# Kernel tuning notes

Hardware: AMD Instinct MI355X
Metric: run time of the kernel (lower is better)

Reference implementation:

```python
import jax, jax.numpy as jnp
import numpy as np

F = 65536          # num_face
W_DIM = 512
PAD = 4096         # zero pad rows appended before gather
LRELU_SLOPE = 0.2
LRELU_GAIN = np.sqrt(2.0).astype(np.float32)  # def_gain of lrelu


def _fc(w, W, b):
    # StyleGAN FullyConnectedLayer: x @ W.T / sqrt(in_features) + bias
    gain = np.float32(1.0 / np.sqrt(W.shape[1]))
    return w @ W.T * gain + b


def _faceconv_gather(x, neigh, is_pad, k):
    # x: [B*F, C]; neigh/is_pad: [B*F, 9]; take first k neighbor slots.
    padded = jnp.concatenate([x, jnp.zeros((PAD, x.shape[1]), x.dtype)], axis=0)
    g = padded[neigh[:, :k]]                      # [B*F, k, C] irregular gather
    return jnp.where(is_pad[:, :k, None], jnp.zeros((), x.dtype), g)


def _modulated_face_conv(g, weight, styles, demodulate):
    # g: [B*F, k, I]; weight: [O, I, 1, k]; styles: [B, I]
    B = styles.shape[0]
    w = weight[None, :, :, 0, :] * styles[:, None, :, None]      # [B, O, I, k]
    if demodulate:
        d = jax.lax.rsqrt(jnp.sum(w * w, axis=(2, 3)) + 1e-8)    # [B, O]
        w = w * d[:, :, None, None]
    gb = g.reshape(B, -1, g.shape[1], g.shape[2])                # [B, F, k, I]
    out = jnp.einsum('bfki,boik->bfo', gb, w)                    # [B, F, O]
    return out.reshape(-1, w.shape[1])


def setup_inputs() -> dict:
    key = jax.random.key(0)
    ks = jax.random.split(key, 12)
    B = 2
    C = 128
    N = B * F
    face_neighborhood = jax.random.randint(ks[0], (N, 9), 0, N + PAD, dtype=jnp.int64)
    face_is_pad = jax.random.randint(ks[1], (N, 9), 0, 10) == 0
    return {
        'face_neighborhood': face_neighborhood,
        'face_is_pad': face_is_pad,
        'ws': jax.random.normal(ks[2], (B, 2, W_DIM), jnp.float32),
        'const': jax.random.normal(ks[3], (F, C), jnp.float32),
        'affine1_W': jax.random.normal(ks[4], (C, W_DIM), jnp.float32),
        'affine1_b': jnp.ones((C,), jnp.float32),
        'weight1': jax.random.normal(ks[5], (C, C, 1, 9), jnp.float32),
        'noise_const': jax.random.normal(ks[6], (F,), jnp.float32),
        'noise_strength': jnp.zeros((1,), jnp.float32),
        'bias1': jnp.zeros((C,), jnp.float32),
        'affine2_W': jax.random.normal(ks[7], (C, W_DIM), jnp.float32),
        'affine2_b': jnp.ones((C,), jnp.float32),
        'weight2': jax.random.normal(ks[8], (3, C, 1, 1), jnp.float32),
        'bias2': jnp.zeros((3,), jnp.float32),
    }


def reference(face_neighborhood, face_is_pad, ws, const, affine1_W, affine1_b,
              weight1, noise_const, noise_strength, bias1, affine2_W, affine2_b,
              weight2, bias2):
    # noise_mode == 'const'
    B = ws.shape[0]
    w0, w1 = ws[:, 0], ws[:, 1]
    x = jnp.tile(const[None], (B, 1, 1)).reshape(B * F, -1)        # [B*F, C]

    # --- SynthesisLayer conv1 ---
    styles = _fc(w0, affine1_W, affine1_b)                         # [B, C]
    noise = jnp.tile(noise_const[None], (B, 1)).reshape(-1, 1) * noise_strength
    g = _faceconv_gather(x, face_neighborhood, face_is_pad, 9)     # [B*F, 9, C]
    x = _modulated_face_conv(g, weight1, styles, demodulate=True)  # [B*F, C]
    x = x + noise
    x = jax.nn.leaky_relu(x + bias1[None, :], LRELU_SLOPE)
    x = jnp.clip(x * LRELU_GAIN, -256.0, 256.0)                    # clamp_gain

    # --- ToRGBLayer ---
    wg = np.float32(1.0 / np.sqrt(weight2.shape[1] * 1))
    styles2 = _fc(w1, affine2_W, affine2_b) * wg
    g2 = _faceconv_gather(x, face_neighborhood, face_is_pad, 1)    # [B*F, 1, C]
    img = _modulated_face_conv(g2, weight2, styles2, demodulate=False)
    img = jnp.clip(img + bias2[None, :], -256.0, 256.0)
    return x, img
```

## Files before the change

kernel.cpp:

```cpp
#include <hip/hip_runtime.h>

typedef unsigned short u16;
typedef __bf16 bf16x8 __attribute__((ext_vector_type(8)));
typedef float f32x4 __attribute__((ext_vector_type(4)));
typedef unsigned short u16x8 __attribute__((ext_vector_type(8)));

#define F_FACES 65536
#define N_FACES 131072
#define C_CH 128
#define WS_W2F 256
#define WS_S1 3328
#define WS_W1 4352
#define WS_CONST 594176
#define XELEMS 16777216

__device__ inline u16 f2bf(float f) {
    unsigned u = __builtin_bit_cast(unsigned, f);
    unsigned r = (u + 0x7fffu + ((u >> 16) & 1u)) >> 16;
    return (u16)r;
}

__device__ inline void gl_lds16(const void* g, void* l) {
    __builtin_amdgcn_global_load_lds(
        (const __attribute__((address_space(1))) void*)g,
        (__attribute__((address_space(3))) void*)l, 16, 0, 0);
}

__global__ __launch_bounds__(256) void k0_styles(
    const float* __restrict__ wsv, const float* __restrict__ a1W, const float* __restrict__ a1b,
    const float* __restrict__ a2W, const float* __restrict__ a2b, const float* __restrict__ w2,
    unsigned char* __restrict__ wsb)
{
    __shared__ float s2s[256];
    int t = threadIdx.x;
    int b = t >> 7, o = t & 127;
    const float* w0r = wsv + (b * 2 + 0) * 512;
    const float* w1r = wsv + (b * 2 + 1) * 512;
    const float* r1 = a1W + o * 512;
    const float* r2 = a2W + o * 512;
    float s1 = 0.f, s2 = 0.f;
    for (int j = 0; j < 512; j += 4) {
        float4 x0 = *(const float4*)(w0r + j);
        float4 x1 = *(const float4*)(w1r + j);
        float4 y1 = *(const float4*)(r1 + j);
        float4 y2 = *(const float4*)(r2 + j);
        s1 += x0.x * y1.x + x0.y * y1.y + x0.z * y1.z + x0.w * y1.w;
        s2 += x1.x * y2.x + x1.y * y2.y + x1.z * y2.z + x1.w * y2.w;
    }
    const float g512 = 0.04419417382415922f;
    const float g128 = 0.08838834764831845f;
    float st1 = s1 * g512 + a1b[o];
    float st2 = (s2 * g512 + a2b[o]) * g128;
    float* wsf = (float*)wsb;
    wsf[WS_S1 / 4 + t] = st1;
    s2s[t] = st2;
    if (t < 64) wsf[t] = 0.f;
    __syncthreads();
#pragma unroll
    for (int r = 0; r < 3; ++r) {
        int id = t + r * 256;
        int b2 = id / 384;
        int rem = id - b2 * 384;
        int o2 = rem >> 7;
        int i = rem & 127;
        wsf[WS_W2F / 4 + id] = w2[o2 * 128 + i] * s2s[b2 * 128 + i];
    }
}

__global__ __launch_bounds__(64) void k0b_fold(
    const float* __restrict__ w1g, const float* __restrict__ s1base, u16* __restrict__ w1out)
{
    int bo = blockIdx.x;
    int b = bo >> 7, o = bo & 127;
    int l = threadIdx.x;
    const float* s1 = s1base + b * 128;
    float sum = 0.f;
    for (int e = l; e < 1152; e += 64) {
        int i = e / 9;
        float w = w1g[o * 1152 + e] * s1[i];
        sum += w * w;
    }
#pragma unroll
    for (int d = 1; d < 64; d <<= 1) sum += __shfl_xor(sum, d);
    float dm = rsqrtf(sum + 1e-8f);
    int i0 = l * 2;
    float sa = s1[i0] * dm, sb = s1[i0 + 1] * dm;
#pragma unroll
    for (int k = 0; k < 9; ++k) {
        float v0 = w1g[(o * 128 + i0) * 9 + k] * sa;
        float v1 = w1g[(o * 128 + i0 + 1) * 9 + k] * sb;
        unsigned pack = (unsigned)f2bf(v0) | ((unsigned)f2bf(v1) << 16);
        *(unsigned*)&w1out[(size_t)(((b * 9 + k) * 128 + o) * 128) + i0] = pack;
    }
}

__global__ __launch_bounds__(256) void k_cvt(
    const float* __restrict__ src, u16* __restrict__ dst)
{
    int t = blockIdx.x * 256 + threadIdx.x;
    int base = t * 8;
    float4 a = *(const float4*)(src + base);
    float4 c = *(const float4*)(src + base + 4);
    u16x8 p;
    p[0] = f2bf(a.x); p[1] = f2bf(a.y); p[2] = f2bf(a.z); p[3] = f2bf(a.w);
    p[4] = f2bf(c.x); p[5] = f2bf(c.y); p[6] = f2bf(c.z); p[7] = f2bf(c.w);
    *(u16x8*)(dst + base) = p;
}

__global__ __launch_bounds__(256, 2) void k1_conv(
    const int* __restrict__ neigh, const int* __restrict__ ispad,
    const float* __restrict__ noise_c, const float* __restrict__ nstr,
    const float* __restrict__ bias1, const unsigned char* __restrict__ wsb,
    float* __restrict__ out)
{
    __shared__ u16 As[128 * 128];
    __shared__ u16 Bs[128 * 128];

    int tid = threadIdx.x;
    int wv = tid >> 6, lane = tid & 63;
    int quad = lane >> 4, l15 = lane & 15;
    int f0 = blockIdx.x * 128;
    int b = f0 >> 16;
    const u16* cst = (const u16*)(wsb + WS_CONST);
    const u16* w1ws = (const u16*)(wsb + WS_W1) + (size_t)b * 147456;
    const char* zp = (const char*)wsb;

    int nidx[8];
    int cg16[8];
    int brow[8];
    int ldso[8];
#pragma unroll
    for (int r = 0; r < 8; ++r) {
        int cid = ((wv * 8 + r) << 6) + lane;
        int row = cid >> 4;
        int slot = cid & 15;
        nidx[r] = (f0 + row) * 9;
        cg16[r] = ((slot ^ (row & 15)) << 4);
        brow[r] = row << 8;
        ldso[r] = (wv * 8 + r) << 10;
    }

    f32x4 acc[4][4] = {};
    int wm = wv & 1, wn = wv >> 1;

    for (int k = 0; k < 9; ++k) {
        __syncthreads();
#pragma unroll
        for (int r = 0; r < 8; ++r) {
            int idx = neigh[nidx[r] + k];
            bool valid = (ispad[nidx[r] + k] == 0) && ((unsigned)idx < 131072u);
            const char* src = valid ? ((const char*)(cst + ((size_t)(idx & 65535) << 7))) : zp;
            gl_lds16(src + cg16[r], (char*)As + ldso[r]);
        }
        const char* bsrc = (const char*)(w1ws + k * 16384);
#pragma unroll
        for (int r = 0; r < 8; ++r) {
            gl_lds16(bsrc + brow[r] + cg16[r], (char*)Bs + ldso[r]);
        }
        __syncthreads();
#pragma unroll
        for (int s = 0; s < 4; ++s) {
            bf16x8 af[4], bfr[4];
#pragma unroll
            for (int mt = 0; mt < 4; ++mt) {
                int face = wm * 64 + mt * 16 + l15;
                int chunk = (s * 4 + quad) ^ (face & 15);
                af[mt] = *reinterpret_cast<const bf16x8*>(&As[face * 128 + chunk * 8]);
            }
#pragma unroll
            for (int nt = 0; nt < 4; ++nt) {
                int o = wn * 64 + nt * 16 + l15;
                int chunk = (s * 4 + quad) ^ (o & 15);
                bfr[nt] = *reinterpret_cast<const bf16x8*>(&Bs[o * 128 + chunk * 8]);
            }
#pragma unroll
            for (int mt = 0; mt < 4; ++mt)
#pragma unroll
                for (int nt = 0; nt < 4; ++nt)
                    acc[mt][nt] = __builtin_amdgcn_mfma_f32_16x16x32_bf16(
                        af[mt], bfr[nt], acc[mt][nt], 0, 0, 0);
        }
    }

    float ns = nstr[0];
    float b1v[4];
#pragma unroll
    for (int nt = 0; nt < 4; ++nt) b1v[nt] = bias1[wn * 64 + nt * 16 + l15];
#pragma unroll
    for (int mt = 0; mt < 4; ++mt) {
#pragma unroll
        for (int r = 0; r < 4; ++r) {
            int face = f0 + wm * 64 + mt * 16 + quad * 4 + r;
            float nz = noise_c[face & 65535] * ns;
#pragma unroll
            for (int nt = 0; nt < 4; ++nt) {
                float v = acc[mt][nt][r] + nz + b1v[nt];
                v = (v > 0.f) ? v : 0.2f * v;
                v *= 1.41421356f;
                v = fminf(fmaxf(v, -256.f), 256.f);
                out[(size_t)face * 128 + wn * 64 + nt * 16 + l15] = v;
            }
        }
    }
}

__global__ __launch_bounds__(256) void k2_img(
    const int* __restrict__ neigh, const int* __restrict__ ispad,
    const float* __restrict__ w2f, const float* __restrict__ bias2,
    const float* __restrict__ xbuf, float* __restrict__ imgout)
{
    int tid = threadIdx.x;
    int wv = tid >> 6, lane = tid & 63;
    int g = lane >> 4, sub = lane & 15;
    int face = blockIdx.x * 16 + wv * 4 + g;
    int b = face >> 16;
    float w[3][8];
#pragma unroll
    for (int o = 0; o < 3; ++o)
#pragma unroll
        for (int j = 0; j < 8; ++j) w[o][j] = w2f[(b * 3 + o) * 128 + sub * 8 + j];
    int idx = neigh[face * 9];
    bool valid = (ispad[face * 9] == 0) && ((unsigned)idx < 131072u);
    float a0 = 0.f, a1 = 0.f, a2 = 0.f;
    if (valid) {
        float4 d0 = *(const float4*)(xbuf + (size_t)idx * 128 + sub * 8);
        float4 d1 = *(const float4*)(xbuf + (size_t)idx * 128 + sub * 8 + 4);
        float f[8] = {d0.x, d0.y, d0.z, d0.w, d1.x, d1.y, d1.z, d1.w};
#pragma unroll
        for (int j = 0; j < 8; ++j) {
            a0 += f[j] * w[0][j];
            a1 += f[j] * w[1][j];
            a2 += f[j] * w[2][j];
        }
    }
#pragma unroll
    for (int d = 1; d < 16; d <<= 1) {
        a0 += __shfl_xor(a0, d);
        a1 += __shfl_xor(a1, d);
        a2 += __shfl_xor(a2, d);
    }
    if (sub < 3) {
        float v = (sub == 0) ? a0 : (sub == 1) ? a1 : a2;
        v += bias2[sub];
        v = fminf(fmaxf(v, -256.f), 256.f);
        imgout[face * 3 + sub] = v;
    }
}

extern "C" void kernel_launch(void* const* d_in, const int* in_sizes, int n_in,
                              void* d_out, int out_size, void* d_ws, size_t ws_size,
                              hipStream_t stream) {
    const int* neigh = (const int*)d_in[0];
    const int* ispad = (const int*)d_in[1];
    const float* wsv = (const float*)d_in[2];
    const float* cst = (const float*)d_in[3];
    const float* a1W = (const float*)d_in[4];
    const float* a1b = (const float*)d_in[5];
    const float* w1g = (const float*)d_in[6];
    const float* noise_c = (const float*)d_in[7];
    const float* nstr = (const float*)d_in[8];
    const float* bias1 = (const float*)d_in[9];
    const float* a2W = (const float*)d_in[10];
    const float* a2b = (const float*)d_in[11];
    const float* w2 = (const float*)d_in[12];
    const float* bias2 = (const float*)d_in[13];
    float* out = (float*)d_out;
    unsigned char* wsb = (unsigned char*)d_ws;

    k0_styles<<<1, 256, 0, stream>>>(wsv, a1W, a1b, a2W, a2b, w2, wsb);
    k0b_fold<<<256, 64, 0, stream>>>(w1g, (const float*)(wsb + WS_S1), (u16*)(wsb + WS_W1));
    k_cvt<<<4096, 256, 0, stream>>>(cst, (u16*)(wsb + WS_CONST));
    k1_conv<<<1024, 256, 0, stream>>>(neigh, ispad, noise_c, nstr, bias1, wsb, out);
    k2_img<<<8192, 256, 0, stream>>>(neigh, ispad, (const float*)(wsb + WS_W2F), bias2,
                                     out, out + XELEMS);
}
```

Baseline: 237.1 us.

## Merge style, demod-fold and const-convert prep kernels into one launch

Folds the three setup kernels (style FC, weight modulation/demodulation fold, const fp32-to-bf16 conversion) into a single kernel that dispatches on block index. The fold blocks each recompute the layer-1 styles themselves, so the serial dependency on a one-block style kernel goes away. This removes two launches and that serial chain, at the cost of redundant style dot products in every fold block. The image kernel also stages the modulated ToRGB weights in shared memory once per block instead of each thread loading 24 values from global memory.

```diff
diff --git a/kernel.cpp b/kernel.cpp
--- a/kernel.cpp
+++ b/kernel.cpp
@@ -7,12 +7,12 @@
 
 #define F_FACES 65536
 #define N_FACES 131072
-#define C_CH 128
 #define WS_W2F 256
-#define WS_S1 3328
 #define WS_W1 4352
 #define WS_CONST 594176
 #define XELEMS 16777216
+#define G512 0.04419417382415922f
+#define G128 0.08838834764831845f
 
 __device__ inline u16 f2bf(float f) {
     unsigned u = __builtin_bit_cast(unsigned, f);
@@ -26,85 +26,96 @@
         (__attribute__((address_space(3))) void*)l, 16, 0, 0);
 }
 
-__global__ __launch_bounds__(256) void k0_styles(
-    const float* __restrict__ wsv, const float* __restrict__ a1W, const float* __restrict__ a1b,
-    const float* __restrict__ a2W, const float* __restrict__ a2b, const float* __restrict__ w2,
+__device__ inline float dot512(const float* a, const float* b) {
+    float s = 0.f;
+    for (int j = 0; j < 512; j += 4) {
+        float4 x = *(const float4*)(a + j);
+        float4 y = *(const float4*)(b + j);
+        s += x.x * y.x + x.y * y.y + x.z * y.z + x.w * y.w;
+    }
+    return s;
+}
+
+__global__ __launch_bounds__(256) void k0_all(
+    const float* __restrict__ cst, const float* __restrict__ wsv,
+    const float* __restrict__ a1W, const float* __restrict__ a1b,
+    const float* __restrict__ a2W, const float* __restrict__ a2b,
+    const float* __restrict__ w1g, const float* __restrict__ w2,
     unsigned char* __restrict__ wsb)
 {
-    __shared__ float s2s[256];
-    int t = threadIdx.x;
-    int b = t >> 7, o = t & 127;
-    const float* w0r = wsv + (b * 2 + 0) * 512;
-    const float* w1r = wsv + (b * 2 + 1) * 512;
-    const float* r1 = a1W + o * 512;
-    const float* r2 = a2W + o * 512;
-    float s1 = 0.f, s2 = 0.f;
-    for (int j = 0; j < 512; j += 4) {
-        float4 x0 = *(const float4*)(w0r + j);
-        float4 x1 = *(const float4*)(w1r + j);
-        float4 y1 = *(const float4*)(r1 + j);
-        float4 y2 = *(const float4*)(r2 + j);
-        s1 += x0.x * y1.x + x0.y * y1.y + x0.z * y1.z + x0.w * y1.w;
-        s2 += x1.x * y2.x + x1.y * y2.y + x1.z * y2.z + x1.w * y2.w;
-    }
-    const float g512 = 0.04419417382415922f;
-    const float g128 = 0.08838834764831845f;
-    float st1 = s1 * g512 + a1b[o];
-    float st2 = (s2 * g512 + a2b[o]) * g128;
-    float* wsf = (float*)wsb;
-    wsf[WS_S1 / 4 + t] = st1;
-    s2s[t] = st2;
-    if (t < 64) wsf[t] = 0.f;
-    __syncthreads();
-#pragma unroll
-    for (int r = 0; r < 3; ++r) {
-        int id = t + r * 256;
-        int b2 = id / 384;
-        int rem = id - b2 * 384;
-        int o2 = rem >> 7;
-        int i = rem & 127;
-        wsf[WS_W2F / 4 + id] = w2[o2 * 128 + i] * s2s[b2 * 128 + i];
-    }
-}
-
-__global__ __launch_bounds__(64) void k0b_fold(
-    const float* __restrict__ w1g, const float* __restrict__ s1base, u16* __restrict__ w1out)
-{
-    int bo = blockIdx.x;
-    int b = bo >> 7, o = bo & 127;
-    int l = threadIdx.x;
-    const float* s1 = s1base + b * 128;
-    float sum = 0.f;
-    for (int e = l; e < 1152; e += 64) {
-        int i = e / 9;
-        float w = w1g[o * 1152 + e] * s1[i];
-        sum += w * w;
-    }
-#pragma unroll
-    for (int d = 1; d < 64; d <<= 1) sum += __shfl_xor(sum, d);
-    float dm = rsqrtf(sum + 1e-8f);
-    int i0 = l * 2;
-    float sa = s1[i0] * dm, sb = s1[i0 + 1] * dm;
-#pragma unroll
-    for (int k = 0; k < 9; ++k) {
-        float v0 = w1g[(o * 128 + i0) * 9 + k] * sa;
-        float v1 = w1g[(o * 128 + i0 + 1) * 9 + k] * sb;
-        unsigned pack = (unsigned)f2bf(v0) | ((unsigned)f2bf(v1) << 16);
-        *(unsigned*)&w1out[(size_t)(((b * 9 + k) * 128 + o) * 128) + i0] = pack;
-    }
-}
-
-__global__ __launch_bounds__(256) void k_cvt(
-    const float* __restrict__ src, u16* __restrict__ dst)
-{
-    int t = blockIdx.x * 256 + threadIdx.x;
-    int base = t * 8;
-    float4 a = *(const float4*)(src + base);
-    float4 c = *(const float4*)(src + base + 4);
-    u16x8 p;
-    p[0] = f2bf(a.x); p[1] = f2bf(a.y); p[2] = f2bf(a.z); p[3] = f2bf(a.w);
-    p[4] = f2bf(c.x); p[5] = f2bf(c.y); p[6] = f2bf(c.z); p[7] = f2bf(c.w);
-    *(u16x8*)(dst + base) = p;
+    __shared__ float sh[392];
+    int bid = blockIdx.x, tid = threadIdx.x;
+    unsigned char* wsb_nr = wsb;
+
+    if (bid < 4096) {
+        int base = (bid * 256 + tid) * 8;
+        const float* src = cst + base;
+        u16* dst = (u16*)(wsb_nr + WS_CONST) + base;
+        float4 a = *(const float4*)(src);
+        float4 c = *(const float4*)(src + 4);
+        u16x8 p;
+        p[0] = f2bf(a.x); p[1] = f2bf(a.y); p[2] = f2bf(a.z); p[3] = f2bf(a.w);
+        p[4] = f2bf(c.x); p[5] = f2bf(c.y); p[6] = f2bf(c.z); p[7] = f2bf(c.w);
+        *(u16x8*)(dst) = p;
+    } else if (bid < 4352) {
+        float* part = sh;
+        float* s1ld = sh + 256;
+        float* wred = sh + 384;
+        int bo = bid - 4096;
+        int b = bo >> 7, o = bo & 127;
+        {
+            int i = tid >> 1, half = tid & 1;
+            const float* x = wsv + (b * 2 + 0) * 512 + half * 256;
+            const float* W = a1W + i * 512 + half * 256;
+            float s = 0.f;
+            for (int j = 0; j < 256; j += 4) {
+                float4 xv = *(const float4*)(x + j);
+                float4 wv = *(const float4*)(W + j);
+                s += xv.x * wv.x + xv.y * wv.y + xv.z * wv.z + xv.w * wv.w;
+            }
+            part[tid] = s;
+        }
+        __syncthreads();
+        if (tid < 128) s1ld[tid] = (part[2 * tid] + part[2 * tid + 1]) * G512 + a1b[tid];
+        __syncthreads();
+        float ds = 0.f;
+        for (int e = tid; e < 1152; e += 256) {
+            int i = e / 9;
+            float w = w1g[o * 1152 + e] * s1ld[i];
+            ds += w * w;
+        }
+#pragma unroll
+        for (int d = 1; d < 64; d <<= 1) ds += __shfl_xor(ds, d);
+        if ((tid & 63) == 0) wred[tid >> 6] = ds;
+        __syncthreads();
+        float dm = rsqrtf(wred[0] + wred[1] + wred[2] + wred[3] + 1e-8f);
+        u16* w1out = (u16*)(wsb_nr + WS_W1);
+#pragma unroll 3
+        for (int p = tid; p < 576; p += 256) {
+            int k = p >> 6, i0 = (p & 63) * 2;
+            float v0 = w1g[(o * 128 + i0) * 9 + k] * s1ld[i0] * dm;
+            float v1 = w1g[(o * 128 + i0 + 1) * 9 + k] * s1ld[i0 + 1] * dm;
+            unsigned pack = (unsigned)f2bf(v0) | ((unsigned)f2bf(v1) << 16);
+            *(unsigned*)&w1out[(size_t)(((b * 9 + k) * 128 + o) * 128) + i0] = pack;
+        }
+    } else {
+        float* s2ld = sh;
+        float* wsf = (float*)wsb_nr;
+        int b2 = tid >> 7, i = tid & 127;
+        float s = dot512(wsv + (b2 * 2 + 1) * 512, a2W + i * 512);
+        s2ld[tid] = (s * G512 + a2b[i]) * G128;
+        if (tid < 64) wsf[tid] = 0.f;
+        __syncthreads();
+#pragma unroll
+        for (int r = 0; r < 3; ++r) {
+            int id = tid + r * 256;
+            int b3 = id / 384;
+            int rem = id - b3 * 384;
+            int o2 = rem >> 7;
+            int ii = rem & 127;
+            wsf[WS_W2F / 4 + id] = w2[o2 * 128 + ii] * s2ld[b3 * 128 + ii];
+        }
+    }
 }
 
 __global__ __launch_bounds__(256, 2) void k1_conv(
@@ -209,16 +220,16 @@
     const float* __restrict__ w2f, const float* __restrict__ bias2,
     const float* __restrict__ xbuf, float* __restrict__ imgout)
 {
+    __shared__ float ws2[768];
     int tid = threadIdx.x;
+    ws2[tid] = w2f[tid];
+    ws2[tid + 256] = w2f[tid + 256];
+    ws2[tid + 512] = w2f[tid + 512];
+    __syncthreads();
     int wv = tid >> 6, lane = tid & 63;
     int g = lane >> 4, sub = lane & 15;
     int face = blockIdx.x * 16 + wv * 4 + g;
     int b = face >> 16;
-    float w[3][8];
-#pragma unroll
-    for (int o = 0; o < 3; ++o)
-#pragma unroll
-        for (int j = 0; j < 8; ++j) w[o][j] = w2f[(b * 3 + o) * 128 + sub * 8 + j];
     int idx = neigh[face * 9];
     bool valid = (ispad[face * 9] == 0) && ((unsigned)idx < 131072u);
     float a0 = 0.f, a1 = 0.f, a2 = 0.f;
@@ -226,11 +237,14 @@
         float4 d0 = *(const float4*)(xbuf + (size_t)idx * 128 + sub * 8);
         float4 d1 = *(const float4*)(xbuf + (size_t)idx * 128 + sub * 8 + 4);
         float f[8] = {d0.x, d0.y, d0.z, d0.w, d1.x, d1.y, d1.z, d1.w};
+        const float* w0 = &ws2[(b * 3 + 0) * 128 + sub * 8];
+        const float* w1 = &ws2[(b * 3 + 1) * 128 + sub * 8];
+        const float* w2p = &ws2[(b * 3 + 2) * 128 + sub * 8];
 #pragma unroll
         for (int j = 0; j < 8; ++j) {
-            a0 += f[j] * w[0][j];
-            a1 += f[j] * w[1][j];
-            a2 += f[j] * w[2][j];
+            a0 += f[j] * w0[j];
+            a1 += f[j] * w1[j];
+            a2 += f[j] * w2p[j];
         }
     }
 #pragma unroll
@@ -267,9 +281,7 @@
     float* out = (float*)d_out;
     unsigned char* wsb = (unsigned char*)d_ws;
 
-    k0_styles<<<1, 256, 0, stream>>>(wsv, a1W, a1b, a2W, a2b, w2, wsb);
-    k0b_fold<<<256, 64, 0, stream>>>(w1g, (const float*)(wsb + WS_S1), (u16*)(wsb + WS_W1));
-    k_cvt<<<4096, 256, 0, stream>>>(cst, (u16*)(wsb + WS_CONST));
+    k0_all<<<4353, 256, 0, stream>>>(cst, wsv, a1W, a1b, a2W, a2b, w1g, w2, wsb);
     k1_conv<<<1024, 256, 0, stream>>>(neigh, ispad, noise_c, nstr, bias1, wsb, out);
     k2_img<<<8192, 256, 0, stream>>>(neigh, ispad, (const float*)(wsb + WS_W2F), bias2,
                                      out, out + XELEMS);
```

Result: slower. 245.7 us (+3.6%).
